# Performance work log

Hardware: AMD Instinct MI355X
Metric: run time of the kernel (lower is better)

Reference implementation:

```python
import jax, jax.numpy as jnp
import numpy as np

N_QUBITS = 20
BATCH = 16


def setup_inputs() -> dict:
    key = jax.random.key(0)
    k1, k2 = jax.random.split(key)
    phi = jax.random.normal(k1, (BATCH, 2 ** N_QUBITS), dtype=jnp.float32)
    thetas = jax.random.normal(k2, (BATCH, N_QUBITS), dtype=jnp.float32)
    return {"phi": phi, "thetas": thetas}


def reference(phi, thetas):
    """Apply per-qubit RX(theta) rotations to the state vector.

    phi: [B, 2**n] real float32 initial amplitudes (cast to complex64).
    thetas: [B, n] rotation angles, qubit 0 = most-significant bit
    (matches torch view([B] + [2]*n) axis ordering, applied sequentially).
    Returns real/imag stacked: [B, 2**n, 2] float32.
    """
    B, S = phi.shape
    n = N_QUBITS
    c = jnp.cos(thetas / 2).astype(jnp.complex64)          # [B, n]
    s = (-1j * jnp.sin(thetas / 2)).astype(jnp.complex64)  # [B, n]
    state = phi.astype(jnp.complex64)                      # [B, S]
    for i in range(n):  # fixed small loop over qubits (butterfly stages)
        left = 2 ** i
        right = S // (2 * left)
        st = state.reshape(B, left, 2, right)
        a = st[:, :, 0, :]
        b = st[:, :, 1, :]
        ci = c[:, i, None, None]
        si = s[:, i, None, None]
        na = ci * a + si * b
        nb = si * a + ci * b
        state = jnp.stack([na, nb], axis=2).reshape(B, S)
    return jnp.stack([state.real, state.imag], axis=-1)
```

## Files before the change

### kernel.cpp

```cpp
#include <hip/hip_runtime.h>

#define NQ 20
#define NS (1 << NQ)

__device__ __forceinline__ float bcast_first(float x) {
    return __int_as_float(__builtin_amdgcn_readfirstlane(__float_as_int(x)));
}

__global__ __launch_bounds__(256) void rx_pass1(
        const float* __restrict__ phi, const float* __restrict__ thetas,
        float2* __restrict__ out) {
    const int lane = threadIdx.x & 63;
    const int W = (blockIdx.x << 2) + (threadIdx.x >> 6);
    const int b = W >> 9;
    const int base = (W & 511) << 11;
    const float* ph = phi + ((size_t)b << NQ) + base;
    float2* op = out + ((size_t)b << NQ) + base;

    float c[11], sv[11];
#pragma unroll
    for (int beta = 0; beta < 11; ++beta) {
        float th = 0.5f * thetas[b * NQ + (NQ - 1 - beta)];
        c[beta]  = bcast_first(cosf(th));
        sv[beta] = bcast_first(sinf(th));
    }

    float2 v[32];
#pragma unroll
    for (int k4 = 0; k4 < 8; ++k4) {
        float4 t = *(const float4*)(ph + (k4 << 8) + (lane << 2));
        v[k4 * 4 + 0] = make_float2(t.x, 0.f);
        v[k4 * 4 + 1] = make_float2(t.y, 0.f);
        v[k4 * 4 + 2] = make_float2(t.z, 0.f);
        v[k4 * 4 + 3] = make_float2(t.w, 0.f);
    }

    const int regbit[5]  = {0, 1, 8, 9, 10};
    const int regmask[5] = {1, 2, 4, 8, 16};
#pragma unroll
    for (int t = 0; t < 5; ++t) {
        const float C = c[regbit[t]], SV = sv[regbit[t]];
        const int m = regmask[t];
#pragma unroll
        for (int r = 0; r < 32; ++r) {
            if (!(r & m)) {
                const int r1 = r | m;
                float2 a = v[r], bb = v[r1];
                v[r]  = make_float2(C * a.x + SV * bb.y, C * a.y - SV * bb.x);
                v[r1] = make_float2(C * bb.x + SV * a.y, C * bb.y - SV * a.x);
            }
        }
    }

#pragma unroll
    for (int t = 0; t < 6; ++t) {
        const float C = c[2 + t], SV = sv[2 + t];
        const int m = 1 << t;
#pragma unroll
        for (int r = 0; r < 32; ++r) {
            float pr = __shfl_xor(v[r].x, m, 64);
            float pi = __shfl_xor(v[r].y, m, 64);
            v[r] = make_float2(C * v[r].x + SV * pi, C * v[r].y - SV * pr);
        }
    }

#pragma unroll
    for (int k4 = 0; k4 < 8; ++k4) {
        float2* dst = op + (k4 << 8) + (lane << 2);
        *(float4*)(dst)     = make_float4(v[k4*4+0].x, v[k4*4+0].y, v[k4*4+1].x, v[k4*4+1].y);
        *(float4*)(dst + 2) = make_float4(v[k4*4+2].x, v[k4*4+2].y, v[k4*4+3].x, v[k4*4+3].y);
    }
}

__global__ __launch_bounds__(256) void rx_pass2(
        const float* __restrict__ thetas, float2* __restrict__ out) {
    const int lane = threadIdx.x & 63;
    const int W = (blockIdx.x << 2) + (threadIdx.x >> 6);
    const int b = W >> 9;
    const int low = ((W & 511) << 2) + (lane & 3);
    const int hl = lane >> 2;
    float2* p = out + ((size_t)b << NQ);

    float c[9], sv[9];
#pragma unroll
    for (int t = 0; t < 9; ++t) {
        float th = 0.5f * thetas[b * NQ + (8 - t)];
        c[t]  = bcast_first(cosf(th));
        sv[t] = bcast_first(sinf(th));
    }

    float2 v[32];
#pragma unroll
    for (int k = 0; k < 32; ++k)
        v[k] = p[(((hl << 5) | k) << 11) + low];

#pragma unroll
    for (int t = 0; t < 5; ++t) {
        const float C = c[t], SV = sv[t];
        const int m = 1 << t;
#pragma unroll
        for (int r = 0; r < 32; ++r) {
            if (!(r & m)) {
                const int r1 = r | m;
                float2 a = v[r], bb = v[r1];
                v[r]  = make_float2(C * a.x + SV * bb.y, C * a.y - SV * bb.x);
                v[r1] = make_float2(C * bb.x + SV * a.y, C * bb.y - SV * a.x);
            }
        }
    }

#pragma unroll
    for (int t = 5; t < 9; ++t) {
        const float C = c[t], SV = sv[t];
        const int m = 4 << (t - 5);
#pragma unroll
        for (int r = 0; r < 32; ++r) {
            float pr = __shfl_xor(v[r].x, m, 64);
            float pi = __shfl_xor(v[r].y, m, 64);
            v[r] = make_float2(C * v[r].x + SV * pi, C * v[r].y - SV * pr);
        }
    }

#pragma unroll
    for (int k = 0; k < 32; ++k)
        p[(((hl << 5) | k) << 11) + low] = v[k];
}

extern "C" void kernel_launch(void* const* d_in, const int* in_sizes, int n_in,
                              void* d_out, int out_size, void* d_ws, size_t ws_size,
                              hipStream_t stream) {
    const float* phi    = (const float*)d_in[0];
    const float* thetas = (const float*)d_in[1];
    float2* out = (float2*)d_out;
    rx_pass1<<<2048, 256, 0, stream>>>(phi, thetas, out);
    rx_pass2<<<2048, 256, 0, stream>>>(thetas, out);
}
```

Measured before the change: 262.6 us.

## Replace cross-lane shuffles with swizzled LDS transposes in both passes

Pass 1 now runs one wave per block and routes its middle qubit stages through a 2048-entry swizzled LDS buffer, so those butterflies are done in registers instead of with paired shuffles. The final stage uses float4 loads and writes with a new contiguous store pattern. Pass 2 becomes 512-thread blocks that stage a 512x16 tile through LDS with float4 coalesced global loads and stores, replacing the old strided 8-byte accesses. This trades shuffle count and uncoalesced traffic for LDS round-trips, extra barriers and higher LDS use per block, which may limit occupancy.

```diff
diff --git a/kernel.cpp b/kernel.cpp
--- a/kernel.cpp
+++ b/kernel.cpp
@@ -1,17 +1,25 @@
 #include <hip/hip_runtime.h>
 
 #define NQ 20
-#define NS (1 << NQ)
 
 __device__ __forceinline__ float bcast_first(float x) {
     return __int_as_float(__builtin_amdgcn_readfirstlane(__float_as_int(x)));
 }
 
-__global__ __launch_bounds__(256) void rx_pass1(
+__device__ __forceinline__ void bfly(float C, float SV, float2& a, float2& b) {
+    float2 na = make_float2(C * a.x + SV * b.y, C * a.y - SV * b.x);
+    float2 nb = make_float2(C * b.x + SV * a.y, C * b.y - SV * a.x);
+    a = na; b = nb;
+}
+
+__device__ __forceinline__ int swz1(int l) { return l ^ (((l >> 7) & 7) << 2); }
+
+__global__ __launch_bounds__(64) void rx_pass1(
         const float* __restrict__ phi, const float* __restrict__ thetas,
         float2* __restrict__ out) {
-    const int lane = threadIdx.x & 63;
-    const int W = (blockIdx.x << 2) + (threadIdx.x >> 6);
+    __shared__ float2 lds[2048];
+    const int lane = threadIdx.x;
+    const int W = blockIdx.x;
     const int b = W >> 9;
     const int base = (W & 511) << 11;
     const float* ph = phi + ((size_t)b << NQ) + base;
@@ -35,95 +43,144 @@
         v[k4 * 4 + 3] = make_float2(t.w, 0.f);
     }
 
-    const int regbit[5]  = {0, 1, 8, 9, 10};
-    const int regmask[5] = {1, 2, 4, 8, 16};
+    const int regbit1[5]  = {0, 1, 8, 9, 10};
+    const int regmask1[5] = {1, 2, 4, 8, 16};
 #pragma unroll
     for (int t = 0; t < 5; ++t) {
-        const float C = c[regbit[t]], SV = sv[regbit[t]];
-        const int m = regmask[t];
+        const float C = c[regbit1[t]], SV = sv[regbit1[t]];
+        const int m = regmask1[t];
 #pragma unroll
-        for (int r = 0; r < 32; ++r) {
-            if (!(r & m)) {
-                const int r1 = r | m;
-                float2 a = v[r], bb = v[r1];
-                v[r]  = make_float2(C * a.x + SV * bb.y, C * a.y - SV * bb.x);
-                v[r1] = make_float2(C * bb.x + SV * a.y, C * bb.y - SV * a.x);
-            }
-        }
-    }
-
-#pragma unroll
-    for (int t = 0; t < 6; ++t) {
-        const float C = c[2 + t], SV = sv[2 + t];
-        const int m = 1 << t;
-#pragma unroll
-        for (int r = 0; r < 32; ++r) {
-            float pr = __shfl_xor(v[r].x, m, 64);
-            float pi = __shfl_xor(v[r].y, m, 64);
-            v[r] = make_float2(C * v[r].x + SV * pi, C * v[r].y - SV * pr);
-        }
+        for (int r = 0; r < 32; ++r)
+            if (!(r & m)) bfly(C, SV, v[r], v[r | m]);
     }
 
 #pragma unroll
     for (int k4 = 0; k4 < 8; ++k4) {
-        float2* dst = op + (k4 << 8) + (lane << 2);
-        *(float4*)(dst)     = make_float4(v[k4*4+0].x, v[k4*4+0].y, v[k4*4+1].x, v[k4*4+1].y);
-        *(float4*)(dst + 2) = make_float4(v[k4*4+2].x, v[k4*4+2].y, v[k4*4+3].x, v[k4*4+3].y);
+        int low0 = (k4 << 8) + (lane << 2);
+        int s0 = swz1(low0);
+        *(float4*)&lds[s0]     = make_float4(v[k4*4+0].x, v[k4*4+0].y, v[k4*4+1].x, v[k4*4+1].y);
+        *(float4*)&lds[s0 + 2] = make_float4(v[k4*4+2].x, v[k4*4+2].y, v[k4*4+3].x, v[k4*4+3].y);
+    }
+    __syncthreads();
+
+    {
+        const int g = lane >> 2, lam = lane & 3;
+        float2 w2[32];
+#pragma unroll
+        for (int r = 0; r < 32; ++r) {
+            int l = (g << 7) | (r << 2) | lam;
+            w2[r] = lds[swz1(l)];
+        }
+#pragma unroll
+        for (int t = 0; t < 5; ++t) {
+            const float C = c[2 + t], SV = sv[2 + t];
+            const int m = 1 << t;
+#pragma unroll
+            for (int r = 0; r < 32; ++r)
+                if (!(r & m)) bfly(C, SV, w2[r], w2[r | m]);
+        }
+#pragma unroll
+        for (int r = 0; r < 32; ++r) {
+            int l = (g << 7) | (r << 2) | lam;
+            lds[swz1(l)] = w2[r];
+        }
+    }
+    __syncthreads();
+
+    float4 u[16];
+#pragma unroll
+    for (int m = 0; m < 16; ++m) {
+        int l0 = (lane << 1) | ((m & 1) << 7) | (((m >> 1) & 1) << 8)
+               | (((m >> 2) & 1) << 9) | (((m >> 3) & 1) << 10);
+        u[m] = *(float4*)&lds[swz1(l0)];
+    }
+    {
+        const float C = c[7], SV = sv[7];
+#pragma unroll
+        for (int m = 0; m < 16; m += 2) {
+            float4 A = u[m], B = u[m + 1];
+            u[m]     = make_float4(C*A.x + SV*B.y, C*A.y - SV*B.x, C*A.z + SV*B.w, C*A.w - SV*B.z);
+            u[m + 1] = make_float4(C*B.x + SV*A.y, C*B.y - SV*A.x, C*B.z + SV*A.w, C*B.w - SV*A.z);
+        }
+    }
+#pragma unroll
+    for (int m = 0; m < 16; ++m) {
+        int l0 = (lane << 1) | ((m & 1) << 7) | (((m >> 1) & 1) << 8)
+               | (((m >> 2) & 1) << 9) | (((m >> 3) & 1) << 10);
+        *(float4*)(op + l0) = u[m];
     }
 }
 
-__global__ __launch_bounds__(256) void rx_pass2(
+__global__ __launch_bounds__(512) void rx_pass2(
         const float* __restrict__ thetas, float2* __restrict__ out) {
-    const int lane = threadIdx.x & 63;
-    const int W = (blockIdx.x << 2) + (threadIdx.x >> 6);
-    const int b = W >> 9;
-    const int low = ((W & 511) << 2) + (lane & 3);
-    const int hl = lane >> 2;
-    float2* p = out + ((size_t)b << NQ);
+    __shared__ float2 buf[8192];
+    const int tid = threadIdx.x;
+    const int lane = tid & 63;
+    const int w = tid >> 6;
+    const int b = blockIdx.x >> 7;
+    const int lb = blockIdx.x & 127;
+    float2* p = out + ((size_t)b << NQ) + (lb << 4);
 
     float c[9], sv[9];
 #pragma unroll
-    for (int t = 0; t < 9; ++t) {
-        float th = 0.5f * thetas[b * NQ + (8 - t)];
-        c[t]  = bcast_first(cosf(th));
-        sv[t] = bcast_first(sinf(th));
+    for (int i = 0; i < 9; ++i) {
+        float th = 0.5f * thetas[b * NQ + (8 - i)];
+        c[i]  = bcast_first(cosf(th));
+        sv[i] = bcast_first(sinf(th));
     }
 
-    float2 v[32];
 #pragma unroll
-    for (int k = 0; k < 32; ++k)
-        v[k] = p[(((hl << 5) | k) << 11) + low];
+    for (int i = 0; i < 8; ++i) {
+        int f = (i << 9) | tid;
+        int h = f >> 3, j = f & 7;
+        float4 t = *(const float4*)(p + h * 2048 + (j << 1));
+        *(float4*)&buf[(h << 4) | (((j << 1) ^ ((h & 7) << 1)))] = t;
+    }
+    __syncthreads();
+
+    const int l = (w << 1) | (lane >> 5);
+    const int g5 = lane & 31;
+    float2 v[16];
+#pragma unroll
+    for (int r = 0; r < 16; ++r) {
+        int h = (r << 5) | g5;
+        v[r] = buf[(h << 4) | (l ^ ((h & 7) << 1))];
+    }
 
 #pragma unroll
     for (int t = 0; t < 5; ++t) {
         const float C = c[t], SV = sv[t];
         const int m = 1 << t;
 #pragma unroll
-        for (int r = 0; r < 32; ++r) {
-            if (!(r & m)) {
-                const int r1 = r | m;
-                float2 a = v[r], bb = v[r1];
-                v[r]  = make_float2(C * a.x + SV * bb.y, C * a.y - SV * bb.x);
-                v[r1] = make_float2(C * bb.x + SV * a.y, C * bb.y - SV * a.x);
-            }
-        }
-    }
-
-#pragma unroll
-    for (int t = 5; t < 9; ++t) {
-        const float C = c[t], SV = sv[t];
-        const int m = 4 << (t - 5);
-#pragma unroll
-        for (int r = 0; r < 32; ++r) {
+        for (int r = 0; r < 16; ++r) {
             float pr = __shfl_xor(v[r].x, m, 64);
             float pi = __shfl_xor(v[r].y, m, 64);
             v[r] = make_float2(C * v[r].x + SV * pi, C * v[r].y - SV * pr);
         }
     }
+#pragma unroll
+    for (int t = 0; t < 4; ++t) {
+        const float C = c[5 + t], SV = sv[5 + t];
+        const int m = 1 << t;
+#pragma unroll
+        for (int r = 0; r < 16; ++r)
+            if (!(r & m)) bfly(C, SV, v[r], v[r | m]);
+    }
 
 #pragma unroll
-    for (int k = 0; k < 32; ++k)
-        p[(((hl << 5) | k) << 11) + low] = v[k];
+    for (int r = 0; r < 16; ++r) {
+        int h = (r << 5) | g5;
+        buf[(h << 4) | (l ^ ((h & 7) << 1))] = v[r];
+    }
+    __syncthreads();
+
+#pragma unroll
+    for (int i = 0; i < 8; ++i) {
+        int f = (i << 9) | tid;
+        int h = f >> 3, j = f & 7;
+        float4 t = *(float4*)&buf[(h << 4) | (((j << 1) ^ ((h & 7) << 1)))];
+        *(float4*)(p + h * 2048 + (j << 1)) = t;
+    }
 }
 
 extern "C" void kernel_launch(void* const* d_in, const int* in_sizes, int n_in,
@@ -132,6 +189,6 @@
     const float* phi    = (const float*)d_in[0];
     const float* thetas = (const float*)d_in[1];
     float2* out = (float2*)d_out;
-    rx_pass1<<<2048, 256, 0, stream>>>(phi, thetas, out);
-    rx_pass2<<<2048, 256, 0, stream>>>(thetas, out);
+    rx_pass1<<<8192, 64, 0, stream>>>(phi, thetas, out);
+    rx_pass2<<<2048, 512, 0, stream>>>(thetas, out);
 }
```

Measured after the change: 245.0 us. 6.7% less time.
